# Kernel optimization log

Hardware: AMD Instinct MI355X
Metric: run time of the kernel (lower is better)

The kernel has to match this reference:

```python
import jax, jax.numpy as jnp
import numpy as np

DIM = 4096
N_HEADS = 32
HEAD_DIM = DIM // N_HEADS
BSZ = 4
SEQLEN = 512
MAX_SEQ = 2048
NEG = -1e9


def _qlinear(x, q, s):
    # int-quantized weight [out,in] dequantized with per-output-channel scale
    w = q.astype(jnp.float32) * s[:, None]
    return jnp.einsum('bsd,od->bso', x, w)


def _apply_rotary(xq, xk, cos, sin):
    # xq,xk: [b,s,h,hd]; cos,sin: [s,hd/2]
    def rot(t):
        b, s, h, d = t.shape
        t = t.reshape(b, s, h, d // 2, 2)
        tr, ti = t[..., 0], t[..., 1]
        c = cos[None, :, None, :]
        sn = sin[None, :, None, :]
        out_r = tr * c - ti * sn
        out_i = tr * sn + ti * c
        return jnp.stack([out_r, out_i], axis=-1).reshape(b, s, h, d)
    return rot(xq), rot(xk)


def setup_inputs() -> dict:
    key = jax.random.key(0)
    ks = jax.random.split(key, 12)
    x = jax.random.normal(ks[0], (BSZ, SEQLEN, DIM), dtype=jnp.float32)
    inv = 1.0 / (10000.0 ** (jnp.arange(0, HEAD_DIM, 2, dtype=jnp.float32) / HEAD_DIM))
    ang = jnp.arange(SEQLEN, dtype=jnp.float32)[:, None] * inv[None, :]
    freqs_cos, freqs_sin = jnp.cos(ang), jnp.sin(ang)
    input_idexes = jnp.arange(SEQLEN, dtype=jnp.int32)  # cache slots being written
    # causal additive mask over full cache: query at position i may attend j <= i
    j = jnp.arange(MAX_SEQ)
    mask = jnp.where(j[None, :] <= input_idexes[:, None], 0.0, NEG).astype(jnp.float32)
    mask = mask[None, None]  # [1,1,S,MAX_SEQ]
    cache_k = jnp.zeros((BSZ, MAX_SEQ, N_HEADS, HEAD_DIM), jnp.float32)
    cache_v = jnp.zeros((BSZ, MAX_SEQ, N_HEADS, HEAD_DIM), jnp.float32)
    SCALE = 2.0 / (127.0 * np.sqrt(DIM))
    def mkw(kq, kscale):
        q = jax.random.randint(kq, (DIM, DIM), -127, 128, dtype=jnp.int32)
        s = jax.random.uniform(kscale, (DIM,), dtype=jnp.float32) * SCALE
        return q, s
    wq_q, wq_s = mkw(ks[1], ks[2])
    wk_q, wk_s = mkw(ks[3], ks[4])
    wv_q, wv_s = mkw(ks[5], ks[6])
    wo_q, wo_s = mkw(ks[7], ks[8])
    return dict(x=x, freqs_cos=freqs_cos, freqs_sin=freqs_sin, mask=mask,
                input_idexes=input_idexes, cache_k=cache_k, cache_v=cache_v,
                wq_q=wq_q, wq_s=wq_s, wk_q=wk_q, wk_s=wk_s,
                wv_q=wv_q, wv_s=wv_s, wo_q=wo_q, wo_s=wo_s)


def reference(x, freqs_cos, freqs_sin, mask, input_idexes, cache_k, cache_v,
              wq_q, wq_s, wk_q, wk_s, wv_q, wv_s, wo_q, wo_s):
    bsz, seqlen, _ = x.shape
    xq = _qlinear(x, wq_q, wq_s).reshape(bsz, seqlen, N_HEADS, HEAD_DIM)
    xk = _qlinear(x, wk_q, wk_s).reshape(bsz, seqlen, N_HEADS, HEAD_DIM)
    xv = _qlinear(x, wv_q, wv_s).reshape(bsz, seqlen, N_HEADS, HEAD_DIM)
    xq, xk = _apply_rotary(xq, xk, freqs_cos, freqs_sin)
    # KV-cache append (index_copy on dim 1)
    cache_k = cache_k.at[:, input_idexes].set(xk)
    cache_v = cache_v.at[:, input_idexes].set(xv)
    # [b,h,q,d] x [b,h,k,d] -> [b,h,q,k]
    scores = jnp.einsum('bqhd,bkhd->bhqk', xq, cache_k) / np.sqrt(HEAD_DIM)
    scores = scores + mask
    probs = jax.nn.softmax(scores.astype(jnp.float32), axis=-1).astype(xq.dtype)
    out = jnp.einsum('bhqk,bkhd->bqhd', probs, cache_v).reshape(bsz, seqlen, -1)
    out = _qlinear(out, wo_q, wo_s)
    return out, (cache_k, cache_v)
```

## Files before the change

kernel.cpp:

```cpp
#include <hip/hip_runtime.h>
#include <cstdint>
#include <cstddef>

typedef __bf16 bf16;
typedef __attribute__((ext_vector_type(8))) __bf16 bf16x8;
typedef __attribute__((ext_vector_type(2))) __bf16 bf16x2;
typedef __attribute__((ext_vector_type(4))) float f32x4;
typedef __attribute__((ext_vector_type(2))) float f32x2;
typedef __attribute__((ext_vector_type(4))) int i32x4;

#define DIMN 4096
#define SEQ 512
#define MAXSEQ 2048
#define NHEAD 32
#define HD 128

#define BM 128
#define BN 128
#define BK 32

__device__ __forceinline__ void gld_lds16(const void* g, void* l) {
  __builtin_amdgcn_global_load_lds(
      (const __attribute__((address_space(1))) unsigned int*)g,
      (__attribute__((address_space(3))) unsigned int*)l, 16, 0, 0);
}

__device__ __forceinline__ void gemm_core(const bf16* Ablk, const bf16* Bblk,
                                          int lda, int ldb, int kmax,
                                          f32x4 acc[4][4], bf16* As, bf16* Bs) {
  const int tid = threadIdx.x;
  const int wave = tid >> 6;
  const int lane = tid & 63;
  const int wm = (wave >> 1) * 64;
  const int wn = (wave & 1) * 64;
  const int lrow = lane & 15;
  const int lkq8 = (lane >> 4) * 8;
  const int srow = wave * 32 + (lane >> 2);
  const int scol = (lane & 3) * 8;
  const bf16* Ag = Ablk + (size_t)srow * lda + scol;
  const bf16* Bg = Bblk + (size_t)srow * ldb + scol;
  bf16* lA = As + wave * 32 * BK;
  bf16* lB = Bs + wave * 32 * BK;

  for (int k0 = 0; k0 < kmax; k0 += BK) {
    __syncthreads();
    gld_lds16(Ag + k0, lA);
    gld_lds16(Ag + k0 + (size_t)16 * lda, lA + 16 * BK);
    gld_lds16(Bg + k0, lB);
    gld_lds16(Bg + k0 + (size_t)16 * ldb, lB + 16 * BK);
    __syncthreads();
    bf16x8 a[4], b[4];
#pragma unroll
    for (int i = 0; i < 4; ++i)
      a[i] = *(const bf16x8*)(As + (wm + i * 16 + lrow) * BK + lkq8);
#pragma unroll
    for (int i = 0; i < 4; ++i)
      b[i] = *(const bf16x8*)(Bs + (wn + i * 16 + lrow) * BK + lkq8);
#pragma unroll
    for (int mi = 0; mi < 4; ++mi)
#pragma unroll
      for (int ni = 0; ni < 4; ++ni)
        acc[mi][ni] = __builtin_amdgcn_mfma_f32_16x16x32_bf16(a[mi], b[ni], acc[mi][ni], 0, 0, 0);
  }
}


#define PBAR do {                              \
    asm volatile("" ::: "memory");             \
    __builtin_amdgcn_sched_barrier(0);         \
    __builtin_amdgcn_s_barrier();              \
    __builtin_amdgcn_sched_barrier(0);         \
    asm volatile("" ::: "memory");             \
  } while (0)

#define STG_A(KT, H, LB) do {                                    \
    const char* _g = Asrc + (KT) * 128 + (H) * 64;               \
    gld_lds16(_g, (LB) + (H) * 8192 + sdst);                     \
  } while (0)
#define STG_B(KT, H, LB) do {                                    \
    const char* _g = Bsrc + (KT) * 128 + (H) * 64;               \
    char* _l = (LB) + 16384 + (H) * 16384 + sdst;                \
    gld_lds16(_g, _l);                                           \
    gld_lds16(_g + (size_t)128 * DIMN, _l + 8192);               \
  } while (0)

#define LDA8(DST, MI, H, LB) \
  DST = *(const i32x4*)((LB) + (H) * 8192 + (MI) * 1024 + aoff)
#define LDB8(DST, NI, H, LB) \
  DST = *(const i32x4*)((LB) + (H) * 16384 + (NI) * 1024 + boff)

#define MFMA16I()                                                           \
    __builtin_amdgcn_s_setprio(1);                                          \
    _Pragma("unroll") for (int _i = 0; _i < 4; ++_i)                        \
      _Pragma("unroll") for (int _n = 0; _n < 4; ++_n)                      \
        acc[_i][_n] = __builtin_amdgcn_mfma_i32_16x16x64_i8(                \
            a[_i], b[_n], acc[_i][_n], 0, 0, 0);                            \
    __builtin_amdgcn_s_setprio(0)

#define TILE2(T, CUR, OTH) do {                                             \
    i32x4 a[4], b[4];                                                       \
                                                      \
    _Pragma("unroll") for (int n = 0; n < 4; ++n) LDB8(b[n], n, 0, CUR);    \
    _Pragma("unroll") for (int i = 0; i < 4; ++i) LDA8(a[i], i, 0, CUR);    \
    STG_A((T) + 1, 1, OTH);                                                 \
    STG_B((T) + 1, 1, OTH);                                                 \
    PBAR; MFMA16I(); PBAR;                                                  \
                                                      \
    _Pragma("unroll") for (int n = 0; n < 4; ++n) LDB8(b[n], n, 1, CUR);    \
    _Pragma("unroll") for (int i = 0; i < 4; ++i) LDA8(a[i], i, 1, CUR);    \
    STG_A((T) + 2, 0, CUR);                                                 \
    STG_B((T) + 2, 0, CUR);                                                 \
    asm volatile("s_waitcnt vmcnt(3)" ::: "memory");                        \
    PBAR; MFMA16I(); PBAR;                                                  \
  } while (0)

__device__ __forceinline__ void gemm128x256_i8(const char* __restrict__ Ablk,
                                               const char* __restrict__ Bblk,
                                               char* lds, i32x4 acc[4][4]) {
  const int tid = threadIdx.x;
  const int wave = tid >> 6, lane = tid & 63;
  const int wm = (wave >> 2) * 64, wn = (wave & 3) * 64;
  const int lrow = lane & 15, q = lane >> 4;
  const int swz = ((q ^ (lrow & 3)) << 4);
  const int aoff = (wm + lrow) * 64 + swz;
  const int boff = 16384 + (wn + lrow) * 64 + swz;
  const int gsw = ((lane & 3) ^ ((lane >> 2) & 3)) << 4;
  const char* Asrc = Ablk + (size_t)(wave * 16 + (lane >> 2)) * DIMN + gsw;
  const char* Bsrc = Bblk + (size_t)(wave * 16 + (lane >> 2)) * DIMN + gsw;
  const int sdst = wave * 1024;
  char* const L0 = lds;
  char* const L1 = lds + 49152;

  STG_A(0, 0, L0); STG_B(0, 0, L0);
  STG_A(0, 1, L0); STG_B(0, 1, L0);
  STG_A(1, 0, L1); STG_B(1, 0, L1);
  asm volatile("s_waitcnt vmcnt(3)" ::: "memory");
  __builtin_amdgcn_sched_barrier(0);
  __builtin_amdgcn_s_barrier();
  __builtin_amdgcn_sched_barrier(0);

  for (int t = 0; t < DIMN / 128; t += 2) {
    TILE2(t, L0, L1);
    TILE2(t + 1, L1, L0);
  }
}

#define ACC_INIT_F(acc)                                 \
  f32x4 acc[4][4];                                      \
  _Pragma("unroll") for (int _i = 0; _i < 4; ++_i)      \
      _Pragma("unroll") for (int _j = 0; _j < 4; ++_j)  \
          acc[_i][_j] = f32x4{0.f, 0.f, 0.f, 0.f};

#define ACC_INIT_I8(acc)                                \
  i32x4 acc[4][4];                                      \
  _Pragma("unroll") for (int _i = 0; _i < 4; ++_i)      \
      _Pragma("unroll") for (int _j = 0; _j < 4; ++_j)  \
          acc[_i][_j] = i32x4{0, 0, 0, 0};

#define EPI_COORDS                                      \
  const int lane = threadIdx.x & 63;                    \
  const int wave = threadIdx.x >> 6;                    \
  const int wm = (wave >> 1) * 64, wn = (wave & 1) * 64;\
  const int cq = (lane >> 4) * 4, cc = lane & 15;

#define EPI8_COORDS                                      \
  const int lane = threadIdx.x & 63;                     \
  const int wave = threadIdx.x >> 6;                     \
  const int wm = (wave >> 2) * 64, wn = (wave & 3) * 64; \
  const int cq = (lane >> 4) * 4, cc = lane & 15;

__global__ __launch_bounds__(256) void k_prep(
    const int* __restrict__ q0, const int* __restrict__ q1,
    const int* __restrict__ q2, const int* __restrict__ q3,
    char* __restrict__ w8, const float* __restrict__ x,
    char* __restrict__ x8, float* __restrict__ xs,
    float* __restrict__ ck, float* __restrict__ cv) {
  __shared__ float red[4];
  const int bx = blockIdx.x;
  const int tid = threadIdx.x;
  if (bx < 16384) {
    const int w = bx >> 12;
    const int* q = (w == 0) ? q0 : (w == 1) ? q1 : (w == 2) ? q2 : q3;
    char* wp = w8 + (size_t)w * 16777216ull;
    size_t i = ((size_t)(bx & 4095) * 256 + tid) * 16;
    const i32x4* qp = (const i32x4*)(q + i);
    i32x4 a = qp[0], b = qp[1], c = qp[2], d = qp[3];
    i32x4 o;
    o[0] = (a[0] & 255) | ((a[1] & 255) << 8) | ((a[2] & 255) << 16) | (a[3] << 24);
    o[1] = (b[0] & 255) | ((b[1] & 255) << 8) | ((b[2] & 255) << 16) | (b[3] << 24);
    o[2] = (c[0] & 255) | ((c[1] & 255) << 8) | ((c[2] & 255) << 16) | (c[3] << 24);
    o[3] = (d[0] & 255) | ((d[1] & 255) << 8) | ((d[2] & 255) << 16) | (d[3] << 24);
    *(i32x4*)(wp + i) = o;
  } else if (bx < 18432) {
    const int row = bx - 16384;
    const float* src = x + (size_t)row * DIMN + tid * 16;
    f32x4 v[4];
#pragma unroll
    for (int j = 0; j < 4; ++j) v[j] = ((const f32x4*)src)[j];
    float am = 0.f;
#pragma unroll
    for (int j = 0; j < 4; ++j)
#pragma unroll
      for (int e = 0; e < 4; ++e) am = fmaxf(am, fabsf(v[j][e]));
#pragma unroll
    for (int off = 32; off; off >>= 1) am = fmaxf(am, __shfl_xor(am, off, 64));
    if ((tid & 63) == 0) red[tid >> 6] = am;
    __syncthreads();
    am = fmaxf(fmaxf(red[0], red[1]), fmaxf(red[2], red[3]));
    const float inv = am > 0.f ? 127.f / am : 0.f;
    i32x4 o;
#pragma unroll
    for (int j = 0; j < 4; ++j) {
      int b0 = (int)rintf(v[j][0] * inv), b1 = (int)rintf(v[j][1] * inv);
      int b2 = (int)rintf(v[j][2] * inv), b3 = (int)rintf(v[j][3] * inv);
      o[j] = (b0 & 255) | ((b1 & 255) << 8) | ((b2 & 255) << 16) | (b3 << 24);
    }
    *(i32x4*)(x8 + (size_t)row * DIMN + tid * 16) = o;
    if (tid == 0) xs[row] = am * (1.f / 127.f);
  } else {
    const int z = bx - 18432;
    const int region = z / 6144;
    const int zoff = z - region * 6144;
    const int b = region >> 1;
    float* base = (region & 1) ? cv : ck;
    char* p = (char*)(base + ((size_t)b * MAXSEQ + SEQ) * DIMN);
    *(f32x4*)(p + (size_t)zoff * 4096 + tid * 16) = f32x4{0.f, 0.f, 0.f, 0.f};
  }
}

__global__ __launch_bounds__(256) void k_quant_attn(const bf16* __restrict__ at,
                                                    char* __restrict__ a8,
                                                    float* __restrict__ as_) {
  __shared__ float red[4];
  const int row = blockIdx.x, tid = threadIdx.x;
  const bf16* src = at + (size_t)row * DIMN + tid * 16;
  bf16x8 h0 = ((const bf16x8*)src)[0], h1 = ((const bf16x8*)src)[1];
  float f[16];
#pragma unroll
  for (int j = 0; j < 8; ++j) { f[j] = (float)h0[j]; f[8 + j] = (float)h1[j]; }
  float am = 0.f;
#pragma unroll
  for (int j = 0; j < 16; ++j) am = fmaxf(am, fabsf(f[j]));
#pragma unroll
  for (int off = 32; off; off >>= 1) am = fmaxf(am, __shfl_xor(am, off, 64));
  if ((tid & 63) == 0) red[tid >> 6] = am;
  __syncthreads();
  am = fmaxf(fmaxf(red[0], red[1]), fmaxf(red[2], red[3]));
  const float inv = am > 0.f ? 127.f / am : 0.f;
  i32x4 o;
#pragma unroll
  for (int j = 0; j < 4; ++j) {
    int b0 = (int)rintf(f[j * 4 + 0] * inv), b1 = (int)rintf(f[j * 4 + 1] * inv);
    int b2 = (int)rintf(f[j * 4 + 2] * inv), b3 = (int)rintf(f[j * 4 + 3] * inv);
    o[j] = (b0 & 255) | ((b1 & 255) << 8) | ((b2 & 255) << 16) | (b3 << 24);
  }
  *(i32x4*)(a8 + (size_t)row * DIMN + tid * 16) = o;
  if (tid == 0) as_[row] = am * (1.f / 127.f);
}

__global__ __launch_bounds__(512, 2) void k_gemm_qkv8(
    const char* __restrict__ X8, const char* __restrict__ W8,
    const float* __restrict__ xs, const float* __restrict__ sq,
    const float* __restrict__ sk, const float* __restrict__ sv,
    const float* __restrict__ fc, const float* __restrict__ fs,
    const int* __restrict__ idx, bf16* __restrict__ qbf,
    bf16* __restrict__ kbf, float* __restrict__ ck, float* __restrict__ cv) {
  __shared__ __align__(16) char lds[98304];
  const int n0 = blockIdx.x * 256;
  const int m0 = blockIdx.y * 128;
  const int z = blockIdx.z;
  const char* W = W8 + (size_t)z * 16777216ull;
  const float* sw = (z == 0) ? sq : (z == 1) ? sk : sv;
  ACC_INIT_I8(acc);
  gemm128x256_i8(X8 + (size_t)m0 * DIMN, W + (size_t)n0 * DIMN, lds, acc);
  EPI8_COORDS;
  if (z < 2) {
    bf16* dst = (z == 0) ? qbf : kbf;
#pragma unroll
    for (int mi = 0; mi < 4; ++mi)
#pragma unroll
      for (int ni = 0; ni < 4; ++ni)
#pragma unroll
        for (int r = 0; r < 4; ++r) {
          const int row = m0 + wm + mi * 16 + cq + r;
          const int col = n0 + wn + ni * 16 + cc;
          const float v = (float)acc[mi][ni][r] * xs[row] * sw[col];
          const float pv = __shfl_xor(v, 1, 64);
          const int s = row & 511, b = row >> 9;
          const int hd = col & 127, h = col >> 7;
          const int d2 = hd >> 1;
          const float c = fc[s * 64 + d2], sn = fs[s * 64 + d2];
          const float o = (col & 1) ? (pv * sn + v * c) : (v * c - pv * sn);
          dst[(((size_t)(b * NHEAD + h)) * SEQ + s) * HD + hd] = (bf16)o;
          if (z == 1) {
            const int pos = idx[s];
            ck[((size_t)b * MAXSEQ + pos) * DIMN + col] = o;
          }
        }
  } else {
#pragma unroll
    for (int mi = 0; mi < 4; ++mi)
#pragma unroll
      for (int ni = 0; ni < 4; ++ni)
#pragma unroll
        for (int r = 0; r < 4; ++r) {
          const int row = m0 + wm + mi * 16 + cq + r;
          const int col = n0 + wn + ni * 16 + cc;
          const int s = row & 511, b = row >> 9;
          cv[((size_t)b * MAXSEQ + s) * DIMN + col] =
              (float)acc[mi][ni][r] * xs[row] * sw[col];
        }
  }
}

__global__ __launch_bounds__(256) void k_vt(const float* __restrict__ cv,
                                            bf16* __restrict__ vt) {
  __shared__ float tile[32][129];
  const int s0 = blockIdx.x * 32;
  const int bh = blockIdx.y;
  const int b = bh >> 5, h = bh & 31;
  const int tid = threadIdx.x;
  const float* src = cv + (size_t)b * MAXSEQ * DIMN + h * HD;
#pragma unroll
  for (int p = 0; p < 16; ++p) {
    const int row = p * 2 + (tid >> 7);
    const int d = tid & 127;
    tile[row][d] = src[(size_t)(s0 + row) * DIMN + d];
  }
  __syncthreads();
  bf16* dst = vt + (size_t)bh * HD * SEQ;
#pragma unroll
  for (int c = 0; c < 16; ++c) {
    const int d = c * 8 + (tid >> 5);
    const int sl = tid & 31;
    dst[(size_t)d * SEQ + s0 + sl] = (bf16)tile[sl][d];
  }
}

__constant__ int g_tm[10] = {0, 1, 1, 2, 2, 2, 3, 3, 3, 3};
__constant__ int g_tn[10] = {0, 0, 1, 0, 1, 2, 0, 1, 2, 3};

__global__ __launch_bounds__(256, 2) void k_gemm_qk(
    const bf16* __restrict__ qb, const bf16* __restrict__ kb,
    bf16* __restrict__ sc) {
  const int m0 = g_tm[blockIdx.x] * BM;
  const int n0 = g_tn[blockIdx.x] * BN;
  const int bh = blockIdx.z;
  __shared__ __align__(16) bf16 As[BM * BK];
  __shared__ __align__(16) bf16 Bs[BN * BK];
  ACC_INIT_F(acc);
  gemm_core(qb + (size_t)bh * SEQ * HD + (size_t)m0 * HD,
            kb + (size_t)bh * SEQ * HD + (size_t)n0 * HD, HD, HD, HD, acc, As, Bs);
  EPI_COORDS;
  bf16* dst = sc + (size_t)bh * SEQ * SEQ;
#pragma unroll
  for (int mi = 0; mi < 4; ++mi)
#pragma unroll
    for (int ni = 0; ni < 4; ++ni)
#pragma unroll
      for (int r = 0; r < 4; ++r) {
        const int row = m0 + wm + mi * 16 + cq + r;
        const int col = n0 + wn + ni * 16 + cc;
        dst[(size_t)row * SEQ + col] = (bf16)(acc[mi][ni][r] * 0.08838834764831845f);
      }
}

__global__ __launch_bounds__(256) void k_softmax(bf16* __restrict__ sc) {
  const int row = blockIdx.x * 4 + (threadIdx.x >> 6);
  const int lane = threadIdx.x & 63;
  const int q = row & 511;
  bf16* p = sc + (size_t)row * SEQ + lane * 8;
  bf16x8 v8 = *(const bf16x8*)p;
  float lv[8];
  float m = -3.0e38f;
#pragma unroll
  for (int j = 0; j < 8; ++j) {
    const int kj = lane * 8 + j;
    lv[j] = (kj <= q) ? (float)v8[j] : -3.0e38f;
    m = fmaxf(m, lv[j]);
  }
#pragma unroll
  for (int off = 32; off; off >>= 1) m = fmaxf(m, __shfl_xor(m, off, 64));
  float e[8];
  float sum = 0.f;
#pragma unroll
  for (int j = 0; j < 8; ++j) {
    e[j] = (lane * 8 + j <= q) ? __expf(lv[j] - m) : 0.f;
    sum += e[j];
  }
#pragma unroll
  for (int off = 32; off; off >>= 1) sum += __shfl_xor(sum, off, 64);
  const float r = 1.f / sum;
  bf16x8 o;
#pragma unroll
  for (int j = 0; j < 8; ++j) o[j] = (bf16)(e[j] * r);
  *(bf16x8*)p = o;
}

__global__ __launch_bounds__(256, 2) void k_gemm_pv(
    const bf16* __restrict__ P, const bf16* __restrict__ vt,
    bf16* __restrict__ attn) {
  const int m0 = blockIdx.y * BM;
  const int bh = blockIdx.z;
  const int kmax = m0 + BM;
  __shared__ __align__(16) bf16 As[BM * BK];
  __shared__ __align__(16) bf16 Bs[BN * BK];
  ACC_INIT_F(acc);
  gemm_core(P + (size_t)bh * SEQ * SEQ + (size_t)m0 * SEQ,
            vt + (size_t)bh * HD * SEQ, SEQ, SEQ, kmax, acc, As, Bs);
  EPI_COORDS;
  const int b = bh >> 5, h = bh & 31;
#pragma unroll
  for (int mi = 0; mi < 4; ++mi)
#pragma unroll
    for (int ni = 0; ni < 4; ++ni)
#pragma unroll
      for (int r = 0; r < 4; ++r) {
        const int row = m0 + wm + mi * 16 + cq + r;
        const int col = wn + ni * 16 + cc;
        attn[((size_t)(b * SEQ + row)) * DIMN + h * HD + col] = (bf16)acc[mi][ni][r];
      }
}

__global__ __launch_bounds__(512, 2) void k_gemm_out8(
    const char* __restrict__ A8, const char* __restrict__ WO8,
    const float* __restrict__ as_, const float* __restrict__ so,
    float* __restrict__ out) {
  __shared__ __align__(16) char lds[98304];
  const int n0 = blockIdx.x * 256;
  const int m0 = blockIdx.y * 128;
  ACC_INIT_I8(acc);
  gemm128x256_i8(A8 + (size_t)m0 * DIMN, WO8 + (size_t)n0 * DIMN, lds, acc);
  EPI8_COORDS;
#pragma unroll
  for (int mi = 0; mi < 4; ++mi)
#pragma unroll
    for (int ni = 0; ni < 4; ++ni)
#pragma unroll
      for (int r = 0; r < 4; ++r) {
        const int row = m0 + wm + mi * 16 + cq + r;
        const int col = n0 + wn + ni * 16 + cc;
        out[(size_t)row * DIMN + col] = (float)acc[mi][ni][r] * as_[row] * so[col];
      }
}

extern "C" void kernel_launch(void* const* d_in, const int* in_sizes, int n_in,
                              void* d_out, int out_size, void* d_ws, size_t ws_size,
                              hipStream_t stream) {
  const float* x = (const float*)d_in[0];
  const float* fc = (const float*)d_in[1];
  const float* fs = (const float*)d_in[2];
  const int* idx = (const int*)d_in[4];
  const int* wq_q = (const int*)d_in[7];
  const int* wk_q = (const int*)d_in[9];
  const int* wv_q = (const int*)d_in[11];
  const int* wo_q = (const int*)d_in[13];
  const float* wq_s = (const float*)d_in[8];
  const float* wk_s = (const float*)d_in[10];
  const float* wv_s = (const float*)d_in[12];
  const float* wo_s = (const float*)d_in[14];

  float* out = (float*)d_out;
  float* ck_out = out + 8388608;
  float* cv_out = ck_out + 33554432;

  char* ws = (char*)d_ws;
  char* W8   = ws;
  char* X8   = ws + 67108864ull;
  float* XS  = (float*)(ws + 75497472ull);
  float* AS  = (float*)(ws + 75513856ull);
  bf16* QBF  = (bf16*)(ws + 83886080ull);
  bf16* KBF  = (bf16*)(ws + 100663296ull);
  bf16* VTB  = (bf16*)(ws + 117440512ull);
  bf16* ATTN = (bf16*)(ws + 134217728ull);
  char* A8   = ws + 150994944ull;
  bf16* SC   = (bf16*)(ws + 167772160ull);

  k_prep<<<dim3(67584), 256, 0, stream>>>(wq_q, wk_q, wv_q, wo_q, W8, x, X8, XS,
                                          ck_out, cv_out);
  k_gemm_qkv8<<<dim3(16, 16, 3), 512, 0, stream>>>(
      X8, W8, XS, wq_s, wk_s, wv_s, fc, fs, idx, QBF, KBF, ck_out, cv_out);
  k_vt<<<dim3(16, 128), 256, 0, stream>>>(cv_out, VTB);
  k_gemm_qk<<<dim3(10, 1, 128), 256, 0, stream>>>(QBF, KBF, SC);
  k_softmax<<<dim3(16384), 256, 0, stream>>>(SC);
  k_gemm_pv<<<dim3(1, 4, 128), 256, 0, stream>>>(SC, VTB, ATTN);
  k_quant_attn<<<dim3(2048), 256, 0, stream>>>(ATTN, A8, AS);
  k_gemm_out8<<<dim3(16, 16), 512, 0, stream>>>(A8, W8 + 50331648ull, AS, wo_s, out);
  (void)in_sizes; (void)n_in; (void)out_size; (void)ws_size;
}
```

Before: 905.2 us.

## Triple-buffer int8 GEMM LDS tiles with full 128-byte row layout

Replaces the double-buffered int8 GEMM mainloop with a three-stage LDS ring, so each K-tile is prefetched two iterations ahead. The LDS layout changes from two 64-byte half-tiles to full 128-byte rows with a new XOR swizzle, and the wait counts and prologue are adjusted to match. LDS per block rises from 96KB to 144KB, which likely drops occupancy from two blocks per CU to one on the 160KB LDS of MI355X. The aim is to hide global-load latency better.

```diff
diff --git a/kernel.cpp b/kernel.cpp
--- a/kernel.cpp
+++ b/kernel.cpp
@@ -73,21 +73,15 @@
     asm volatile("" ::: "memory");             \
   } while (0)
 
-#define STG_A(KT, H, LB) do {                                    \
-    const char* _g = Asrc + (KT) * 128 + (H) * 64;               \
-    gld_lds16(_g, (LB) + (H) * 8192 + sdst);                     \
-  } while (0)
-#define STG_B(KT, H, LB) do {                                    \
-    const char* _g = Bsrc + (KT) * 128 + (H) * 64;               \
-    char* _l = (LB) + 16384 + (H) * 16384 + sdst;                \
-    gld_lds16(_g, _l);                                           \
-    gld_lds16(_g + (size_t)128 * DIMN, _l + 8192);               \
-  } while (0)
+#define STG_A(KT, C, LB) \
+  gld_lds16(Asrc + (KT) * 128 + (size_t)(C) * 64 * DIMN, (LB) + (C) * 8192 + sdst)
+#define STG_B(KT, C, LB) \
+  gld_lds16(Bsrc + (KT) * 128 + (size_t)(C) * 64 * DIMN, (LB) + 16384 + (C) * 8192 + sdst)
 
 #define LDA8(DST, MI, H, LB) \
-  DST = *(const i32x4*)((LB) + (H) * 8192 + (MI) * 1024 + aoff)
+  DST = *(const i32x4*)((LB) + (MI) * 2048 + aoff + ((H) ? g1off : g0off))
 #define LDB8(DST, NI, H, LB) \
-  DST = *(const i32x4*)((LB) + (H) * 16384 + (NI) * 1024 + boff)
+  DST = *(const i32x4*)((LB) + 16384 + (NI) * 2048 + boff + ((H) ? g1off : g0off))
 
 #define MFMA16I()                                                           \
     __builtin_amdgcn_s_setprio(1);                                          \
@@ -97,20 +91,22 @@
             a[_i], b[_n], acc[_i][_n], 0, 0, 0);                            \
     __builtin_amdgcn_s_setprio(0)
 
-#define TILE2(T, CUR, OTH) do {                                             \
+#define TILE3(T, CUR, STG) do {                                             \
     i32x4 a[4], b[4];                                                       \
                                                       \
     _Pragma("unroll") for (int n = 0; n < 4; ++n) LDB8(b[n], n, 0, CUR);    \
     _Pragma("unroll") for (int i = 0; i < 4; ++i) LDA8(a[i], i, 0, CUR);    \
-    STG_A((T) + 1, 1, OTH);                                                 \
-    STG_B((T) + 1, 1, OTH);                                                 \
+    STG_B((T) + 2, 0, STG);                                                 \
+    STG_B((T) + 2, 1, STG);                                                 \
+    STG_A((T) + 2, 0, STG);                                                 \
     PBAR; MFMA16I(); PBAR;                                                  \
                                                       \
     _Pragma("unroll") for (int n = 0; n < 4; ++n) LDB8(b[n], n, 1, CUR);    \
     _Pragma("unroll") for (int i = 0; i < 4; ++i) LDA8(a[i], i, 1, CUR);    \
-    STG_A((T) + 2, 0, CUR);                                                 \
-    STG_B((T) + 2, 0, CUR);                                                 \
-    asm volatile("s_waitcnt vmcnt(3)" ::: "memory");                        \
+    STG_B((T) + 2, 2, STG);                                                 \
+    STG_B((T) + 2, 3, STG);                                                 \
+    STG_A((T) + 2, 1, STG);                                                 \
+    asm volatile("s_waitcnt vmcnt(6)" ::: "memory");                        \
     PBAR; MFMA16I(); PBAR;                                                  \
   } while (0)
 
@@ -121,28 +117,36 @@
   const int wave = tid >> 6, lane = tid & 63;
   const int wm = (wave >> 2) * 64, wn = (wave & 3) * 64;
   const int lrow = lane & 15, q = lane >> 4;
-  const int swz = ((q ^ (lrow & 3)) << 4);
-  const int aoff = (wm + lrow) * 64 + swz;
-  const int boff = 16384 + (wn + lrow) * 64 + swz;
-  const int gsw = ((lane & 3) ^ ((lane >> 2) & 3)) << 4;
-  const char* Asrc = Ablk + (size_t)(wave * 16 + (lane >> 2)) * DIMN + gsw;
-  const char* Bsrc = Bblk + (size_t)(wave * 16 + (lane >> 2)) * DIMN + gsw;
+  const int qx = q ^ (lrow & 3);
+  const int hbit = (lrow >> 2) & 1;
+  const int g0off = (((hbit) << 2) | qx) << 4;
+  const int g1off = (((hbit ^ 1) << 2) | qx) << 4;
+  const int aoff = (wm + lrow) * 128;
+  const int boff = (wn + lrow) * 128;
+  const int gsw = ((lane & 7) ^ (lane >> 3)) << 4;
+  const char* Asrc = Ablk + (size_t)(wave * 8 + (lane >> 3)) * DIMN + gsw;
+  const char* Bsrc = Bblk + (size_t)(wave * 8 + (lane >> 3)) * DIMN + gsw;
   const int sdst = wave * 1024;
   char* const L0 = lds;
   char* const L1 = lds + 49152;
-
-  STG_A(0, 0, L0); STG_B(0, 0, L0);
-  STG_A(0, 1, L0); STG_B(0, 1, L0);
-  STG_A(1, 0, L1); STG_B(1, 0, L1);
-  asm volatile("s_waitcnt vmcnt(3)" ::: "memory");
+  char* const L2 = lds + 98304;
+
+  STG_A(0, 0, L0); STG_A(0, 1, L0);
+  STG_B(0, 0, L0); STG_B(0, 1, L0); STG_B(0, 2, L0); STG_B(0, 3, L0);
+  STG_A(1, 0, L1); STG_A(1, 1, L1);
+  STG_B(1, 0, L1); STG_B(1, 1, L1); STG_B(1, 2, L1); STG_B(1, 3, L1);
+  asm volatile("s_waitcnt vmcnt(6)" ::: "memory");
   __builtin_amdgcn_sched_barrier(0);
   __builtin_amdgcn_s_barrier();
   __builtin_amdgcn_sched_barrier(0);
 
-  for (int t = 0; t < DIMN / 128; t += 2) {
-    TILE2(t, L0, L1);
-    TILE2(t + 1, L1, L0);
-  }
+  for (int t = 0; t < 30; t += 3) {
+    TILE3(t, L0, L2);
+    TILE3(t + 1, L1, L0);
+    TILE3(t + 2, L2, L1);
+  }
+  TILE3(30, L0, L2);
+  TILE3(31, L1, L0);
 }
 
 #define ACC_INIT_F(acc)                                 \
@@ -265,7 +269,7 @@
     const float* __restrict__ fc, const float* __restrict__ fs,
     const int* __restrict__ idx, bf16* __restrict__ qbf,
     bf16* __restrict__ kbf, float* __restrict__ ck, float* __restrict__ cv) {
-  __shared__ __align__(16) char lds[98304];
+  __shared__ __align__(16) char lds[147456];
   const int n0 = blockIdx.x * 256;
   const int m0 = blockIdx.y * 128;
   const int z = blockIdx.z;
@@ -426,7 +430,7 @@
     const char* __restrict__ A8, const char* __restrict__ WO8,
     const float* __restrict__ as_, const float* __restrict__ so,
     float* __restrict__ out) {
-  __shared__ __align__(16) char lds[98304];
+  __shared__ __align__(16) char lds[147456];
   const int n0 = blockIdx.x * 256;
   const int m0 = blockIdx.y * 128;
   ACC_INIT_I8(acc);
```

Measured after the change: 866.5 us. 4.3% less time.
